# Performance work log

Hardware: AMD Instinct MI355X
Metric: run time of the kernel (lower is better)

## Reference

```python
import jax, jax.numpy as jnp
import numpy as np

B, S, D, H = 4, 1024, 1024, 16
DK = D // H  # 64


def setup_inputs() -> dict:
    key = jax.random.key(0)
    ks = jax.random.split(key, 12)
    scale = 0.02
    inp = {
        "query": jax.random.normal(ks[0], (B, S, D), jnp.float32),
        "key": jax.random.normal(ks[1], (B, S, D), jnp.float32),
        "value": jax.random.normal(ks[2], (B, S, D), jnp.float32),
        "mask": jax.random.randint(ks[3], (B, 1, S, S), 0, 2, jnp.int32),
        "wq": jax.random.normal(ks[4], (D, D), jnp.float32) * scale,
        "bq": jnp.zeros((D,), jnp.float32),
        "wk": jax.random.normal(ks[5], (D, D), jnp.float32) * scale,
        "bk": jnp.zeros((D,), jnp.float32),
        "wv": jax.random.normal(ks[6], (D, D), jnp.float32) * scale,
        "bv": jnp.zeros((D,), jnp.float32),
        "wo": jax.random.normal(ks[7], (D, D), jnp.float32) * scale,
        "bo": jnp.zeros((D,), jnp.float32),
    }
    return inp


def reference(query, key, value, mask, wq, bq, wk, bk, wv, bv, wo, bo):
    # Linear projections (torch Linear: x @ W.T + b)
    q = query @ wq.T + bq
    k = key @ wk.T + bk
    v = value @ wv.T + bv
    # [B,S,D] -> [B,H,S,DK]
    q = q.reshape(B, S, H, DK).transpose(0, 2, 1, 3)
    k = k.reshape(B, S, H, DK).transpose(0, 2, 1, 3)
    v = v.reshape(B, S, H, DK).transpose(0, 2, 1, 3)
    # scaled dot-product attention with mask (-1e9 where mask==0)
    scores = jnp.einsum('bhqd,bhkd->bhqk', q, k) / jnp.sqrt(jnp.float32(DK))
    scores = jnp.where(mask == 0, jnp.float32(-1e9), scores)
    attn = jax.nn.softmax(scores, axis=-1)  # dropout p=0.0 -> identity
    x = jnp.einsum('bhqk,bhkd->bhqd', attn, v)
    # [B,H,S,DK] -> [B,S,D]
    x = x.transpose(0, 2, 1, 3).reshape(B, S, D)
    return x @ wo.T + bo
```

## Files before the change

kernel.cpp:

```cpp
#include <hip/hip_runtime.h>


typedef __attribute__((ext_vector_type(8))) short short8;
typedef __attribute__((ext_vector_type(4))) float f32x4;
typedef __attribute__((ext_vector_type(4))) unsigned short u16x4;
typedef unsigned short u16;
typedef unsigned long long u64;

#define SCALE_Q 0.180336880f

__device__ __forceinline__ u16 f2bf(float f) {
    unsigned u = __float_as_uint(f);
    return (u16)((u + 0x7FFFu + ((u >> 16) & 1u)) >> 16);
}
__device__ __forceinline__ u16 f2bf_fast(float f) {
    return (u16)((__float_as_uint(f) + 0x8000u) >> 16);
}
__device__ __forceinline__ float bf2f(u16 v) {
    return __uint_as_float((unsigned)v << 16);
}

__device__ __forceinline__ void gl_lds16(const u16* g, u16* l) {
    __builtin_amdgcn_global_load_lds(
        (__attribute__((address_space(1))) void*)g,
        (__attribute__((address_space(3))) void*)l, 16, 0, 0);
}

__global__ __launch_bounds__(256) void prep(
    const float* __restrict__ q, const float* __restrict__ k,
    const float* __restrict__ v, const float* __restrict__ wq,
    const float* __restrict__ wk, const float* __restrict__ wv,
    const float* __restrict__ wo, const int* __restrict__ mask,
    u16* __restrict__ xq, u16* __restrict__ xk, u16* __restrict__ xv,
    u16* __restrict__ wqb, u16* __restrict__ wkb, u16* __restrict__ wvb,
    u16* __restrict__ wob, u64* __restrict__ bits) {
    int bid = blockIdx.x;
    if (bid < 16384) {
        const float* src; u16* dst; int i;
        if (bid < 12288) {
            int chunk = bid >> 12;
            int off = bid & 4095;
            src = (chunk == 0) ? q : ((chunk == 1) ? k : v);
            dst = (chunk == 0) ? xq : ((chunk == 1) ? xk : xv);
            i = off * 256 + threadIdx.x;
        } else {
            int wb = bid - 12288;
            int chunk = wb >> 10;
            int off = wb & 1023;
            src = (chunk == 0) ? wq : ((chunk == 1) ? wk : ((chunk == 2) ? wv : wo));
            dst = (chunk == 0) ? wqb : ((chunk == 1) ? wkb : ((chunk == 2) ? wvb : wob));
            i = off * 256 + threadIdx.x;
        }
        f32x4 val = ((const f32x4*)src)[i];
        u16x4 r;
        r.x = f2bf(val.x); r.y = f2bf(val.y); r.z = f2bf(val.z); r.w = f2bf(val.w);
        ((u16x4*)dst)[i] = r;
    } else {
        int mb = bid - 16384;
        int wid = threadIdx.x >> 6, lane = threadIdx.x & 63;
        int base = mb * 1024 + wid * 256;
        int b = mb >> 10, qrow = mb & 1023;
        #pragma unroll
        for (int j = 0; j < 4; ++j) {
            u64 bal = __ballot(mask[base + j * 64 + lane] != 0);
            int kt = wid * 4 + j;
            if (lane == 0) bits[(size_t)(b * 16 + kt) * 1024 + qrow] = bal;
        }
    }
}

__global__ __launch_bounds__(256, 3) void gemm_qkv(
    const u16* __restrict__ Aq, const u16* __restrict__ Ak, const u16* __restrict__ Av,
    const u16* __restrict__ Wq, const u16* __restrict__ Wk, const u16* __restrict__ Wv,
    const float* __restrict__ bq, const float* __restrict__ bk, const float* __restrict__ bv,
    u16* __restrict__ Qo, u16* __restrict__ Ko, u16* __restrict__ VTo) {
    __shared__ __align__(16) u16 As[128 * 64];
    __shared__ __align__(16) u16 Bs[128 * 64];
    const int id = blockIdx.x;
    const int n0 = (id / 96) * 128;
    const int pm = id % 96;
    const int p = pm >> 5;
    const int m0 = (pm & 31) * 128;
    const u16* A = (p == 0) ? Aq : ((p == 1) ? Ak : Av);
    const u16* W = (p == 0) ? Wq : ((p == 1) ? Wk : Wv);
    const float* bias = (p == 0) ? bq : ((p == 1) ? bk : bv);

    const int t = threadIdx.x;
    const int lane = t & 63;
    const int wid = t >> 6;
    const int l15 = lane & 15;
    const int quad = lane >> 4;
    const int wm = (wid & 1) * 64;
    const int wn = (wid >> 1) * 64;
    const int r8 = lane >> 3, gr = lane & 7;
    const int gsw = (gr ^ r8) * 8;

    f32x4 acc[4][4];
    #pragma unroll
    for (int i = 0; i < 4; ++i)
        #pragma unroll
        for (int j = 0; j < 4; ++j) acc[i][j] = (f32x4){0.f, 0.f, 0.f, 0.f};

    for (int kt = 0; kt < 1024; kt += 64) {
        __syncthreads();
        #pragma unroll
        for (int c = 0; c < 8; ++c) {
            int call = wid * 8 + c;
            if (call < 16) {
                int rb = call * 8;
                gl_lds16(&A[(size_t)(m0 + rb + r8) * 1024 + kt + gsw], &As[rb * 64]);
            } else {
                int rb = (call - 16) * 8;
                gl_lds16(&W[(size_t)(n0 + rb + r8) * 1024 + kt + gsw], &Bs[rb * 64]);
            }
        }
        __syncthreads();
        #pragma unroll
        for (int ks = 0; ks < 2; ++ks) {
            short8 af[4], bf[4];
            #pragma unroll
            for (int i = 0; i < 4; ++i) {
                int mr = wm + i * 16 + l15;
                af[i] = *(const short8*)&As[mr * 64 + (((ks << 2) + quad) ^ (mr & 7)) * 8];
                int nr = wn + i * 16 + l15;
                bf[i] = *(const short8*)&Bs[nr * 64 + (((ks << 2) + quad) ^ (nr & 7)) * 8];
            }
            #pragma unroll
            for (int mi = 0; mi < 4; ++mi)
                #pragma unroll
                for (int ni = 0; ni < 4; ++ni)
                    acc[mi][ni] = __builtin_amdgcn_mfma_f32_16x16x32_bf16(
                        af[mi], bf[ni], acc[mi][ni], 0, 0, 0);
        }
    }

    u16* dst01 = (p == 0) ? Qo : Ko;
    const float qs = (p == 0) ? SCALE_Q : 1.0f;
    #pragma unroll
    for (int mi = 0; mi < 4; ++mi) {
        #pragma unroll
        for (int ni = 0; ni < 4; ++ni) {
            int col = n0 + wn + ni * 16 + l15;
            int h = col >> 6, dk = col & 63;
            float bcol = bias[col];
            if (p < 2) {
                #pragma unroll
                for (int r = 0; r < 4; ++r) {
                    int row = m0 + wm + mi * 16 + quad * 4 + r;
                    int bb = row >> 10, s = row & 1023;
                    dst01[(size_t)((bb * 16 + h) * 1024 + s) * 64 + dk] =
                        f2bf((acc[mi][ni][r] + bcol) * qs);
                }
            } else {
                int row0 = m0 + wm + mi * 16 + quad * 4;
                int bb = row0 >> 10, s0 = row0 & 1023;
                u64 pk = 0;
                #pragma unroll
                for (int r = 0; r < 4; ++r)
                    pk |= (u64)f2bf(acc[mi][ni][r] + bcol) << (16 * r);
                *(u64*)&VTo[(size_t)((bb * 16 + h) * 64 + dk) * 1024 + s0] = pk;
            }
        }
    }
}

__global__ __launch_bounds__(256, 3) void gemm_out(
    const u16* __restrict__ X, const u16* __restrict__ Wo,
    const float* __restrict__ bo, float* __restrict__ out) {
    __shared__ __align__(16) u16 As[64 * 64];
    __shared__ __align__(16) u16 Bs[128 * 64];
    const int id = blockIdx.x;
    const int n0 = (id >> 6) * 128;
    const int m0 = (id & 63) * 64;
    const int t = threadIdx.x;
    const int lane = t & 63;
    const int wid = t >> 6;
    const int l15 = lane & 15;
    const int quad = lane >> 4;
    const int wm = (wid & 1) * 32;
    const int wn = (wid >> 1) * 64;
    const int r8 = lane >> 3, gr = lane & 7;
    const int gsw = (gr ^ r8) * 8;

    f32x4 acc[2][4];
    #pragma unroll
    for (int i = 0; i < 2; ++i)
        #pragma unroll
        for (int j = 0; j < 4; ++j) acc[i][j] = (f32x4){0.f, 0.f, 0.f, 0.f};

    for (int kt = 0; kt < 1024; kt += 64) {
        __syncthreads();
        #pragma unroll
        for (int c = 0; c < 6; ++c) {
            int call = wid * 6 + c;
            if (call < 8) {
                int rb = call * 8;
                gl_lds16(&X[(size_t)(m0 + rb + r8) * 1024 + kt + gsw], &As[rb * 64]);
            } else {
                int rb = (call - 8) * 8;
                gl_lds16(&Wo[(size_t)(n0 + rb + r8) * 1024 + kt + gsw], &Bs[rb * 64]);
            }
        }
        __syncthreads();
        #pragma unroll
        for (int ks = 0; ks < 2; ++ks) {
            short8 af[2], bf[4];
            #pragma unroll
            for (int i = 0; i < 2; ++i) {
                int mr = wm + i * 16 + l15;
                af[i] = *(const short8*)&As[mr * 64 + (((ks << 2) + quad) ^ (mr & 7)) * 8];
            }
            #pragma unroll
            for (int j = 0; j < 4; ++j) {
                int nr = wn + j * 16 + l15;
                bf[j] = *(const short8*)&Bs[nr * 64 + (((ks << 2) + quad) ^ (nr & 7)) * 8];
            }
            #pragma unroll
            for (int mi = 0; mi < 2; ++mi)
                #pragma unroll
                for (int ni = 0; ni < 4; ++ni)
                    acc[mi][ni] = __builtin_amdgcn_mfma_f32_16x16x32_bf16(
                        af[mi], bf[ni], acc[mi][ni], 0, 0, 0);
        }
    }

    #pragma unroll
    for (int mi = 0; mi < 2; ++mi) {
        #pragma unroll
        for (int ni = 0; ni < 4; ++ni) {
            int col = n0 + wn + ni * 16 + l15;
            float bcol = bo[col];
            #pragma unroll
            for (int r = 0; r < 4; ++r) {
                int row = m0 + wm + mi * 16 + quad * 4 + r;
                out[(size_t)row * 1024 + col] = acc[mi][ni][r] + bcol;
            }
        }
    }
}

__global__ __launch_bounds__(256) void attn_kernel(
    const u16* __restrict__ Q, const u16* __restrict__ K, const u16* __restrict__ VT,
    const u64* __restrict__ mbits, u16* __restrict__ O, float* __restrict__ L) {
    __shared__ __align__(16) u16 Ks[64 * 64];
    __shared__ __align__(16) u16 Vs[64 * 64];
    __shared__ __align__(16) u16 Ps[4][32 * 72];

    const int qt = blockIdx.x;
    const int h = blockIdx.y;
    const int b = blockIdx.z >> 1;
    const int half = blockIdx.z & 1;
    const int t = threadIdx.x;
    const int lane = t & 63;
    const int wid = t >> 6;
    const int l15 = lane & 15;
    const int quad = lane >> 4;
    const int qw = qt * 128 + wid * 32;
    const int sr = t >> 3;
    const int sc = t & 7;
    const int ktg0 = half * 8;

    const size_t headoff = (size_t)(b * 16 + h) * 1024 * 64;
    const u16* Qh = Q + headoff;
    const u16* Kh = K + headoff;
    const u16* Vh = VT + headoff;

    short8 qf[2][2];
    #pragma unroll
    for (int g = 0; g < 2; ++g)
        #pragma unroll
        for (int ks = 0; ks < 2; ++ks)
            qf[g][ks] = *(const short8*)&Qh[(size_t)(qw + g * 16 + l15) * 64 + ks * 32 + quad * 8];

    f32x4 o_acc[2][4];
    #pragma unroll
    for (int g = 0; g < 2; ++g)
        #pragma unroll
        for (int j = 0; j < 4; ++j) o_acc[g][j] = (f32x4){0.f, 0.f, 0.f, 0.f};
    float lacc[2] = {0.f, 0.f};

    const u64* mbase = &mbits[(size_t)(b * 16) * 1024 + qw + l15];

    short8 kpre[2], vpre[2];
    #pragma unroll
    for (int p = 0; p < 2; ++p) {
        int r = p * 32 + sr;
        kpre[p] = *(const short8*)&Kh[(size_t)(ktg0 * 64 + r) * 64 + sc * 8];
        vpre[p] = *(const short8*)&Vh[(size_t)r * 1024 + ktg0 * 64 + sc * 8];
    }

    for (int kt = 0; kt < 8; ++kt) {
        __syncthreads();
        #pragma unroll
        for (int p = 0; p < 2; ++p) {
            int r = p * 32 + sr;
            int gl = sc ^ (r & 7);
            *(short8*)&Ks[r * 64 + gl * 8] = kpre[p];
            *(short8*)&Vs[r * 64 + gl * 8] = vpre[p];
        }
        __syncthreads();

        if (kt < 7) {
            int kvn = (ktg0 + kt + 1) * 64;
            #pragma unroll
            for (int p = 0; p < 2; ++p) {
                int r = p * 32 + sr;
                kpre[p] = *(const short8*)&Kh[(size_t)(kvn + r) * 64 + sc * 8];
                vpre[p] = *(const short8*)&Vh[(size_t)r * 1024 + kvn + sc * 8];
            }
        }

        f32x4 sacc[2][4];
        #pragma unroll
        for (int g = 0; g < 2; ++g)
            #pragma unroll
            for (int j = 0; j < 4; ++j) sacc[g][j] = (f32x4){0.f, 0.f, 0.f, 0.f};
        #pragma unroll
        for (int ks = 0; ks < 2; ++ks) {
            #pragma unroll
            for (int mi = 0; mi < 4; ++mi) {
                int n = mi * 16 + l15;
                short8 kf = *(const short8*)&Ks[n * 64 + (((ks << 2) + quad) ^ (n & 7)) * 8];
                sacc[0][mi] = __builtin_amdgcn_mfma_f32_16x16x32_bf16(kf, qf[0][ks], sacc[0][mi], 0, 0, 0);
                sacc[1][mi] = __builtin_amdgcn_mfma_f32_16x16x32_bf16(kf, qf[1][ks], sacc[1][mi], 0, 0, 0);
            }
        }

        #pragma unroll
        for (int g = 0; g < 2; ++g) {
            u64 w = mbase[(size_t)(ktg0 + kt) * 1024 + g * 16];
            unsigned t0 = (unsigned)(w >> (quad * 4));
            unsigned t1 = (unsigned)(w >> (quad * 4 + 32));
            #pragma unroll
            for (int mi = 0; mi < 4; ++mi) {
                unsigned sel = (mi & 2) ? t1 : t0;
                sel >>= (mi & 1) * 16;
                u64 pk = 0;
                #pragma unroll
                for (int r = 0; r < 4; ++r) {
                    float p = __builtin_amdgcn_exp2f(sacc[g][mi][r]);
                    p = ((sel >> r) & 1u) ? p : 0.f;
                    lacc[g] += p;
                    pk |= (u64)f2bf_fast(p) << (16 * r);
                }
                *(u64*)&Ps[wid][(g * 16 + l15) * 72 + mi * 16 + quad * 4] = pk;
            }
        }

        #pragma unroll
        for (int ks = 0; ks < 2; ++ks) {
            short8 pf0 = *(const short8*)&Ps[wid][(size_t)l15 * 72 + ks * 32 + quad * 8];
            short8 pf1 = *(const short8*)&Ps[wid][(size_t)(16 + l15) * 72 + ks * 32 + quad * 8];
            #pragma unroll
            for (int j = 0; j < 4; ++j) {
                int d = j * 16 + l15;
                short8 vf = *(const short8*)&Vs[d * 64 + (((ks << 2) + quad) ^ (d & 7)) * 8];
                o_acc[0][j] = __builtin_amdgcn_mfma_f32_16x16x32_bf16(pf0, vf, o_acc[0][j], 0, 0, 0);
                o_acc[1][j] = __builtin_amdgcn_mfma_f32_16x16x32_bf16(pf1, vf, o_acc[1][j], 0, 0, 0);
            }
        }
    }

    u16* Oh = O + (size_t)half * 4194304;
    float* Lh = L + (size_t)half * 65536;
    #pragma unroll
    for (int g = 0; g < 2; ++g) {
        float l = lacc[g];
        l += __shfl_xor(l, 16);
        l += __shfl_xor(l, 32);
        if (lane < 16)
            Lh[(size_t)(b * 16 + h) * 1024 + qw + g * 16 + lane] = l;
        #pragma unroll
        for (int r = 0; r < 4; ++r) {
            int qrow = qw + g * 16 + quad * 4 + r;
            #pragma unroll
            for (int ni = 0; ni < 4; ++ni) {
                Oh[(size_t)(b * 1024 + qrow) * 1024 + h * 64 + ni * 16 + l15] =
                    f2bf(o_acc[g][ni][r]);
            }
        }
    }
}

__global__ __launch_bounds__(256) void merge_halves(
    const u16* __restrict__ O, const float* __restrict__ L, u16* __restrict__ X) {
    int i = (blockIdx.x * 256 + threadIdx.x) * 8;
    int b = i >> 20, s = (i >> 10) & 1023, c = i & 1023, h = c >> 6;
    short8 o0 = *(const short8*)&O[i];
    short8 o1 = *(const short8*)&O[4194304 + i];
    size_t li = (size_t)(b * 16 + h) * 1024 + s;
    float inv = 1.0f / (L[li] + L[65536 + li]);
    short8 r;
    #pragma unroll
    for (int j = 0; j < 8; ++j) {
        float x = (bf2f((u16)o0[j]) + bf2f((u16)o1[j])) * inv;
        r[j] = (short)f2bf(x);
    }
    *(short8*)&X[i] = r;
}

extern "C" void kernel_launch(void* const* d_in, const int* in_sizes, int n_in,
                              void* d_out, int out_size, void* d_ws, size_t ws_size,
                              hipStream_t stream) {
    const float* query = (const float*)d_in[0];
    const float* key_ = (const float*)d_in[1];
    const float* value = (const float*)d_in[2];
    const int* mask = (const int*)d_in[3];
    const float* wq = (const float*)d_in[4];
    const float* bq = (const float*)d_in[5];
    const float* wk = (const float*)d_in[6];
    const float* bk = (const float*)d_in[7];
    const float* wv = (const float*)d_in[8];
    const float* bv = (const float*)d_in[9];
    const float* wo = (const float*)d_in[10];
    const float* bo = (const float*)d_in[11];
    float* out = (float*)d_out;

    char* ws = (char*)d_ws;
    const size_t XB = (size_t)4096 * 1024 * 2;
    const size_t WB = (size_t)1024 * 1024 * 2;
    u16* xq = (u16*)(ws);
    u16* xk = (u16*)(ws + XB);
    u16* xv = (u16*)(ws + 2 * XB);
    u16* wqb = (u16*)(ws + 3 * XB);
    u16* wkb = (u16*)(ws + 3 * XB + WB);
    u16* wvb = (u16*)(ws + 3 * XB + 2 * WB);
    u16* wob = (u16*)(ws + 3 * XB + 3 * WB);
    u16* Qb = (u16*)(ws + 3 * XB + 4 * WB);
    u16* Kb = (u16*)(ws + 4 * XB + 4 * WB);
    u16* VTb = (u16*)(ws + 5 * XB + 4 * WB);
    u64* bits = (u64*)(ws + 6 * XB + 4 * WB);
    float* Lbuf = (float*)(ws + 6 * XB + 4 * WB + (512 << 10));
    u16* Opart = xk;
    u16* Xattn = xq;

    prep<<<20480, 256, 0, stream>>>(query, key_, value, wq, wk, wv, wo, mask,
                                    xq, xk, xv, wqb, wkb, wvb, wob, bits);
    gemm_qkv<<<768, 256, 0, stream>>>(xq, xk, xv, wqb, wkb, wvb,
                                      bq, bk, bv, Qb, Kb, VTb);
    attn_kernel<<<dim3(8, 16, 8), 256, 0, stream>>>(Qb, Kb, VTb, bits, Opart, Lbuf);
    merge_halves<<<2048, 256, 0, stream>>>(Opart, Lbuf, Xattn);
    gemm_out<<<512, 256, 0, stream>>>(Xattn, wob, bo, out);
}
```

Measured before the change: 233.8 us.

## Load K/V fragments directly from global memory and remap attention blocks across XCDs

The attention kernel drops its shared-memory staging of K and V tiles, along with the two barriers per iteration. Each wave now loads its MFMA operand fragments straight from global memory and relies on cache reuse across the four waves. The grid becomes 1D with a block-index remap that groups the 8 query tiles of one head/half together (bid&7 spread), so blocks on the same XCD share K/V in L2. Packing P to bf16 is also rewritten with paired conversions. The risk is redundant global/L1 traffic, since every wave reloads the same K/V, and higher load latency without prefetch.

Result: slower. 255.5 us (+9.3%).

```diff
diff --git a/kernel.cpp b/kernel.cpp
--- a/kernel.cpp
+++ b/kernel.cpp
@@ -12,9 +12,6 @@
 __device__ __forceinline__ u16 f2bf(float f) {
     unsigned u = __float_as_uint(f);
     return (u16)((u + 0x7FFFu + ((u >> 16) & 1u)) >> 16);
-}
-__device__ __forceinline__ u16 f2bf_fast(float f) {
-    return (u16)((__float_as_uint(f) + 0x8000u) >> 16);
 }
 __device__ __forceinline__ float bf2f(u16 v) {
     return __uint_as_float((unsigned)v << 16);
@@ -242,22 +239,23 @@
 __global__ __launch_bounds__(256) void attn_kernel(
     const u16* __restrict__ Q, const u16* __restrict__ K, const u16* __restrict__ VT,
     const u64* __restrict__ mbits, u16* __restrict__ O, float* __restrict__ L) {
-    __shared__ __align__(16) u16 Ks[64 * 64];
-    __shared__ __align__(16) u16 Vs[64 * 64];
     __shared__ __align__(16) u16 Ps[4][32 * 72];
 
-    const int qt = blockIdx.x;
-    const int h = blockIdx.y;
-    const int b = blockIdx.z >> 1;
-    const int half = blockIdx.z & 1;
+    const int bid = blockIdx.x;
+    const int work = (bid & 7) * 128 + (bid >> 3);
+    const int qt = work & 7;
+    const int combo = work >> 3;
+    const int h = combo & 15;
+    const int bh = combo >> 4;
+    const int b = bh >> 1;
+    const int half = bh & 1;
+
     const int t = threadIdx.x;
     const int lane = t & 63;
     const int wid = t >> 6;
     const int l15 = lane & 15;
     const int quad = lane >> 4;
     const int qw = qt * 128 + wid * 32;
-    const int sr = t >> 3;
-    const int sc = t & 7;
     const int ktg0 = half * 8;
 
     const size_t headoff = (size_t)(b * 16 + h) * 1024 * 64;
@@ -279,36 +277,13 @@
         for (int j = 0; j < 4; ++j) o_acc[g][j] = (f32x4){0.f, 0.f, 0.f, 0.f};
     float lacc[2] = {0.f, 0.f};
 
-    const u64* mbase = &mbits[(size_t)(b * 16) * 1024 + qw + l15];
-
-    short8 kpre[2], vpre[2];
-    #pragma unroll
-    for (int p = 0; p < 2; ++p) {
-        int r = p * 32 + sr;
-        kpre[p] = *(const short8*)&Kh[(size_t)(ktg0 * 64 + r) * 64 + sc * 8];
-        vpre[p] = *(const short8*)&Vh[(size_t)r * 1024 + ktg0 * 64 + sc * 8];
-    }
+    const u16* kp = Kh + (size_t)(ktg0 * 64 + l15) * 64 + quad * 8;
+    const u16* vp = Vh + (size_t)l15 * 1024 + ktg0 * 64 + quad * 8;
+    const u64* mp = mbits + (size_t)(b * 16 + ktg0) * 1024 + qw + l15;
 
     for (int kt = 0; kt < 8; ++kt) {
-        __syncthreads();
-        #pragma unroll
-        for (int p = 0; p < 2; ++p) {
-            int r = p * 32 + sr;
-            int gl = sc ^ (r & 7);
-            *(short8*)&Ks[r * 64 + gl * 8] = kpre[p];
-            *(short8*)&Vs[r * 64 + gl * 8] = vpre[p];
-        }
-        __syncthreads();
-
-        if (kt < 7) {
-            int kvn = (ktg0 + kt + 1) * 64;
-            #pragma unroll
-            for (int p = 0; p < 2; ++p) {
-                int r = p * 32 + sr;
-                kpre[p] = *(const short8*)&Kh[(size_t)(kvn + r) * 64 + sc * 8];
-                vpre[p] = *(const short8*)&Vh[(size_t)r * 1024 + kvn + sc * 8];
-            }
-        }
+        u64 w0 = mp[0];
+        u64 w1 = mp[16];
 
         f32x4 sacc[2][4];
         #pragma unroll
@@ -319,31 +294,42 @@
         for (int ks = 0; ks < 2; ++ks) {
             #pragma unroll
             for (int mi = 0; mi < 4; ++mi) {
-                int n = mi * 16 + l15;
-                short8 kf = *(const short8*)&Ks[n * 64 + (((ks << 2) + quad) ^ (n & 7)) * 8];
+                short8 kf = *(const short8*)&kp[mi * 1024 + ks * 32];
                 sacc[0][mi] = __builtin_amdgcn_mfma_f32_16x16x32_bf16(kf, qf[0][ks], sacc[0][mi], 0, 0, 0);
                 sacc[1][mi] = __builtin_amdgcn_mfma_f32_16x16x32_bf16(kf, qf[1][ks], sacc[1][mi], 0, 0, 0);
             }
         }
 
+        short8 vf[2][4];
+        #pragma unroll
+        for (int ks = 0; ks < 2; ++ks)
+            #pragma unroll
+            for (int j = 0; j < 4; ++j)
+                vf[ks][j] = *(const short8*)&vp[(size_t)j * 16384 + ks * 32];
+
         #pragma unroll
         for (int g = 0; g < 2; ++g) {
-            u64 w = mbase[(size_t)(ktg0 + kt) * 1024 + g * 16];
+            u64 w = g ? w1 : w0;
             unsigned t0 = (unsigned)(w >> (quad * 4));
             unsigned t1 = (unsigned)(w >> (quad * 4 + 32));
             #pragma unroll
             for (int mi = 0; mi < 4; ++mi) {
                 unsigned sel = (mi & 2) ? t1 : t0;
                 sel >>= (mi & 1) * 16;
-                u64 pk = 0;
+                unsigned pw[2];
                 #pragma unroll
-                for (int r = 0; r < 4; ++r) {
-                    float p = __builtin_amdgcn_exp2f(sacc[g][mi][r]);
-                    p = ((sel >> r) & 1u) ? p : 0.f;
-                    lacc[g] += p;
-                    pk |= (u64)f2bf_fast(p) << (16 * r);
+                for (int pr = 0; pr < 2; ++pr) {
+                    float p0 = __builtin_amdgcn_exp2f(sacc[g][mi][pr * 2]);
+                    float p1 = __builtin_amdgcn_exp2f(sacc[g][mi][pr * 2 + 1]);
+                    p0 = ((sel >> (pr * 2)) & 1u) ? p0 : 0.f;
+                    p1 = ((sel >> (pr * 2 + 1)) & 1u) ? p1 : 0.f;
+                    lacc[g] += p0;
+                    lacc[g] += p1;
+                    pw[pr] = ((__float_as_uint(p0) + 0x8000u) >> 16) |
+                             ((__float_as_uint(p1) + 0x8000u) & 0xFFFF0000u);
                 }
-                *(u64*)&Ps[wid][(g * 16 + l15) * 72 + mi * 16 + quad * 4] = pk;
+                *(u64*)&Ps[wid][(g * 16 + l15) * 72 + mi * 16 + quad * 4] =
+                    (u64)pw[0] | ((u64)pw[1] << 32);
             }
         }
 
@@ -353,12 +339,14 @@
             short8 pf1 = *(const short8*)&Ps[wid][(size_t)(16 + l15) * 72 + ks * 32 + quad * 8];
             #pragma unroll
             for (int j = 0; j < 4; ++j) {
-                int d = j * 16 + l15;
-                short8 vf = *(const short8*)&Vs[d * 64 + (((ks << 2) + quad) ^ (d & 7)) * 8];
-                o_acc[0][j] = __builtin_amdgcn_mfma_f32_16x16x32_bf16(pf0, vf, o_acc[0][j], 0, 0, 0);
-                o_acc[1][j] = __builtin_amdgcn_mfma_f32_16x16x32_bf16(pf1, vf, o_acc[1][j], 0, 0, 0);
-            }
-        }
+                o_acc[0][j] = __builtin_amdgcn_mfma_f32_16x16x32_bf16(pf0, vf[ks][j], o_acc[0][j], 0, 0, 0);
+                o_acc[1][j] = __builtin_amdgcn_mfma_f32_16x16x32_bf16(pf1, vf[ks][j], o_acc[1][j], 0, 0, 0);
+            }
+        }
+
+        kp += 4096;
+        vp += 64;
+        mp += 1024;
     }
 
     u16* Oh = O + (size_t)half * 4194304;
@@ -438,7 +426,7 @@
                                     xq, xk, xv, wqb, wkb, wvb, wob, bits);
     gemm_qkv<<<768, 256, 0, stream>>>(xq, xk, xv, wqb, wkb, wvb,
                                       bq, bk, bv, Qb, Kb, VTb);
-    attn_kernel<<<dim3(8, 16, 8), 256, 0, stream>>>(Qb, Kb, VTb, bits, Opart, Lbuf);
+    attn_kernel<<<1024, 256, 0, stream>>>(Qb, Kb, VTb, bits, Opart, Lbuf);
     merge_halves<<<2048, 256, 0, stream>>>(Opart, Lbuf, Xattn);
     gemm_out<<<512, 256, 0, stream>>>(Xattn, wob, bo, out);
 }
```
